# Kernel optimization log

Measured on AMD Instinct MI355X. Metric: run time of the kernel, lower is better.

## Reference

```python
import jax, jax.numpy as jnp
import numpy as np

SIGMA = 0.1
B = 1.0
SPATIAL_WEIGHT = 0.5
EPS = 1e-5


def setup_inputs() -> dict:
    key = jax.random.key(0)
    k1, k2 = jax.random.split(key)
    N, C, H, W = 2, 256, 64, 64
    I_features = jax.random.normal(k1, (N, C, H, W), dtype=jnp.float32)
    T_features = jax.random.normal(k2, (N, C, H, W), dtype=jnp.float32)
    return {"I_features": I_features, "T_features": T_features}


def _calc_cx(raw):
    # raw: [N, P_T, H, W]; min + exp-softmax over the target-patch axis (axis=1)
    mn = jnp.min(raw, axis=1, keepdims=True)
    rel = raw / (mn + EPS)
    w = jnp.exp((B - rel) / SIGMA)
    return w / jnp.sum(w, axis=1, keepdims=True)


def reference(I_features, T_features):
    N, C, H, W = I_features.shape
    P = H * W

    # ---- spatial branch: L2 distances on a normalized meshgrid (C=2) ----
    rows = jnp.arange(H, dtype=jnp.float32) / (H + 1)
    cols = jnp.arange(W, dtype=jnp.float32) / (W + 1)
    grid = jnp.stack(jnp.meshgrid(rows, cols, indexing="ij"))  # [2, H, W]
    g = grid.reshape(2, P)                                      # [2, P]
    sq = jnp.sum(g * g, axis=0)                                 # [P]
    d = sq[:, None] + sq[None, :] - 2.0 * (g.T @ g)             # [P_I, P_T]
    d = jnp.clip(d, 0.0)
    raw_sp = d.T.reshape(1, P, H, W)  # [1, P_T, H, W]; identical per sample
    cx_sp = _calc_cx(raw_sp)

    # ---- feature branch: cosine similarity via centered, L2-normed feats ----
    meanT = jnp.mean(T_features, axis=(0, 2, 3), keepdims=True)
    Ic = I_features - meanT
    Tc = T_features - meanT
    In = Ic / jnp.linalg.norm(Ic, axis=1, keepdims=True)
    Tn = Tc / jnp.linalg.norm(Tc, axis=1, keepdims=True)
    Iv = In.reshape(N, C, P)
    Tv = Tn.reshape(N, C, P)
    dot = jnp.einsum("ncq,ncp->nqp", Tv, Iv)  # [N, P_T, P_I]
    raw_feat = ((1.0 - dot) / 2.0).reshape(N, P, H, W)
    cx_feat = _calc_cx(raw_feat)

    # ---- combine, max over I positions, mean over T patches, -log, mean ----
    cx = (1.0 - SPATIAL_WEIGHT) * cx_feat + SPATIAL_WEIGHT * cx_sp  # [N,P,H,W]
    m = jnp.max(cx, axis=(2, 3))  # [N, P]
    m = jnp.mean(m, axis=1)       # [N]
    return jnp.mean(-jnp.log(m))
```

## Files before the change

### kernel.cpp

```cpp
#include <hip/hip_runtime.h>
#include <math.h>

#define PP 4096
#define CC 256
#define NN 2
#define NSTEP 16

typedef __attribute__((ext_vector_type(4))) float f32x4;

__device__ __forceinline__ void gld_lds16(const char* g, char* l) {
    __builtin_amdgcn_global_load_lds(
        (const __attribute__((address_space(1))) unsigned int*)g,
        (__attribute__((address_space(3))) unsigned int*)l, 16, 0, 0);
}


__global__ __launch_bounds__(256) void mean_kernel(const float* __restrict__ T,
                                                   float* __restrict__ meanT,
                                                   float* __restrict__ loss_acc) {
    int c = blockIdx.x, tid = threadIdx.x;
    float s = 0.f;
    for (int n = 0; n < NN; n++) {
        const float4* Tc = (const float4*)&T[(size_t)(n * CC + c) * PP];
        for (int g = 0; g < 4; g++) {
            float4 v = Tc[tid + g * 256];
            s += (v.x + v.y) + (v.z + v.w);
        }
    }
    __shared__ float red[256];
    red[tid] = s; __syncthreads();
    for (int st = 128; st > 0; st >>= 1) {
        if (tid < st) red[tid] += red[tid + st];
        __syncthreads();
    }
    if (tid == 0) meanT[c] = red[0] * (1.0f / (NN * PP));
    if (blockIdx.x == 0 && tid < NN) loss_acc[tid] = 0.f;
}

__global__ __launch_bounds__(256) void normalize_kernel(const float* __restrict__ I,
                                                        const float* __restrict__ T,
                                                        const float* __restrict__ meanT,
                                                        char* __restrict__ InT,
                                                        char* __restrict__ TnT) {
    int pc = blockIdx.x * 32;
    int n = blockIdx.y;
    int which = blockIdx.z;
    const float* X = which ? T : I;
    char* Y = which ? TnT : InT;

    __shared__ float tile[CC][36];
    __shared__ float red[32][32];
    __shared__ float invn[32];

    int tid = threadIdx.x;
    int pl4 = tid & 7, c0 = tid >> 3;
    float sq0 = 0.f, sq1 = 0.f, sq2 = 0.f, sq3 = 0.f;
    for (int c = c0; c < CC; c += 32) {
        float m = meanT[c];
        float4 v = *(const float4*)&X[(size_t)(n * CC + c) * PP + pc + pl4 * 4];
        v.x -= m; v.y -= m; v.z -= m; v.w -= m;
        *(float4*)&tile[c][pl4 * 4] = v;
        sq0 += v.x * v.x; sq1 += v.y * v.y; sq2 += v.z * v.z; sq3 += v.w * v.w;
    }
    red[c0][pl4 * 4 + 0] = sq0;
    red[c0][pl4 * 4 + 1] = sq1;
    red[c0][pl4 * 4 + 2] = sq2;
    red[c0][pl4 * 4 + 3] = sq3;
    __syncthreads();
    if (tid < 32) {
        float s = 0.f;
        for (int k = 0; k < 32; k++) s += red[k][tid];
        invn[tid] = 1.0f / sqrtf(s);
    }
    __syncthreads();
    for (int pass = 0; pass < 8; pass++) {
        int r = pass * 4 + (tid >> 6);
        int c4 = (tid & 63) * 4;
        float in = invn[r];
        float v0 = tile[c4 + 0][r] * in;
        float v1 = tile[c4 + 1][r] * in;
        float v2 = tile[c4 + 2][r] * in;
        float v3 = tile[c4 + 3][r] * in;
        int w = __builtin_amdgcn_cvt_pk_fp8_f32(v0, v1, 0, false);
        w = __builtin_amdgcn_cvt_pk_fp8_f32(v2, v3, w, true);
        *(unsigned*)&Y[(size_t)(n * PP + pc + r) * CC + c4] = (unsigned)w;
    }
}

__global__ __launch_bounds__(512) void cx_strip(const char* __restrict__ TnT,
                                                const char* __restrict__ InT,
                                                float* __restrict__ loss_acc) {
    const int strip = blockIdx.x;
    const int n = blockIdx.y;
    const int p0 = strip * 32;
    const char* __restrict__ Ab = TnT + (size_t)n * PP * CC;
    const char* __restrict__ Bb = InT + (size_t)n * PP * CC + (size_t)p0 * CC;

    __shared__ __align__(16) char Aw[8][2][8192];
    __shared__ __align__(16) char Bsm[8192];
    __shared__ float redw[8][32];
    __shared__ float inv2s[32];
    __shared__ float dwl[32];

    const int tid = threadIdx.x;
    const int l = tid & 63, wv = tid >> 6;
    const int lm = l & 15, quad = l >> 4;
    const int lr4 = l >> 4;
    const int sl = l & 15;

#define STAGE_A(qs, b)                                                       \
    {                                                                        \
        const char* sbase_ = Ab + ((size_t)(qs) * 256 + wv * 32) * 256;      \
        char* dbase_ = &Aw[wv][b][0];                                        \
        _Pragma("unroll")                                                    \
        for (int g_ = 0; g_ < 8; g_++) {                                     \
            int row_ = g_ * 4 + lr4;                                         \
            gld_lds16(sbase_ + row_ * 256 + ((sl ^ (row_ & 15)) * 16),       \
                      dbase_ + g_ * 1024);                                   \
        }                                                                    \
    }

    {
        int rB = wv * 4 + lr4;
        gld_lds16(Bb + rB * 256 + ((sl ^ (rB & 15)) * 16), &Bsm[wv * 1024]);
    }
    STAGE_A(0, 0);
    __syncthreads();

    long bf[2][8];
#pragma unroll
    for (int ct = 0; ct < 2; ct++)
#pragma unroll
        for (int ks = 0; ks < 8; ks++) {
            int g8 = ks * 4 + quad;
            int row = ct * 16 + lm;
            bf[ct][ks] = *(const long*)&Bsm[row * 256 +
                          (((g8 >> 1) ^ (row & 15)) * 16) + (g8 & 1) * 8];
        }

    float cm[2] = {3.4e38f, 3.4e38f};
    float inv2[2] = {0.f, 0.f};
    float ss[2] = {0.f, 0.f};
    const int qd = p0 >> 8;
    const int wd = (p0 >> 5) & 7;

#pragma unroll 1
    for (int pass = 0; pass < 2; pass++) {
        if (pass == 1) STAGE_A(0, 0);
#pragma unroll 1
        for (int qs = 0; qs < NSTEP; qs++) {
            if (qs < NSTEP - 1) {
                STAGE_A(qs + 1, (qs + 1) & 1);
                asm volatile("s_waitcnt vmcnt(8)" ::: "memory");
            } else {
                asm volatile("s_waitcnt vmcnt(0)" ::: "memory");
            }
            __builtin_amdgcn_sched_barrier(0);

            const char* Ac = &Aw[wv][qs & 1][0];
            f32x4 acc[2][2] = {};
#pragma unroll
            for (int ks = 0; ks < 8; ks++) {
                const int off = (((ks * 2 + (quad >> 1)) ^ lm) * 16) + (quad & 1) * 8;
                long a[2];
#pragma unroll
                for (int i = 0; i < 2; i++)
                    a[i] = *(const long*)&Ac[(i * 16 + lm) * 256 + off];
#pragma unroll
                for (int i = 0; i < 2; i++)
#pragma unroll
                    for (int ct = 0; ct < 2; ct++)
                        acc[i][ct] = __builtin_amdgcn_mfma_f32_16x16x32_fp8_fp8(
                            a[i], bf[ct][ks], acc[i][ct], 0, 0, 0);
            }
            if (pass == 0) {
#pragma unroll
                for (int ct = 0; ct < 2; ct++)
#pragma unroll
                    for (int i = 0; i < 2; i++)
#pragma unroll
                        for (int e = 0; e < 4; e++)
                            cm[ct] = fminf(cm[ct], (1.0f - acc[i][ct][e]) * 0.5f);
            } else {
                const bool dstep = (qs == qd) && (wv == wd);
#pragma unroll
                for (int ct = 0; ct < 2; ct++) {
                    float s2 = 0.f;
#pragma unroll
                    for (int i = 0; i < 2; i++)
#pragma unroll
                        for (int e = 0; e < 4; e++) {
                            float raw = (1.0f - acc[i][ct][e]) * 0.5f;
                            float w = exp2f(fmaf(raw, -inv2[ct], 14.4269504f));
                            s2 += w;
                            if (dstep && (i * 16 + quad * 4 + e == ct * 16 + lm))
                                dwl[ct * 16 + lm] = w;
                        }
                    ss[ct] += s2;
                }
            }
        }

        if (pass == 0) {
#pragma unroll
            for (int ct = 0; ct < 2; ct++) {
                cm[ct] = fminf(cm[ct], __shfl_xor(cm[ct], 16));
                cm[ct] = fminf(cm[ct], __shfl_xor(cm[ct], 32));
                if (quad == 0) redw[wv][ct * 16 + lm] = cm[ct];
            }
            __syncthreads();
            if (tid < 32) {
                float m = redw[0][tid];
#pragma unroll
                for (int w2 = 1; w2 < 8; w2++) m = fminf(m, redw[w2][tid]);
                inv2s[tid] = 14.4269504f / (m + 1e-5f);
            }
            __syncthreads();
            inv2[0] = inv2s[lm];
            inv2[1] = inv2s[16 + lm];
        }
    }

#pragma unroll
    for (int ct = 0; ct < 2; ct++) {
        ss[ct] += __shfl_xor(ss[ct], 16);
        ss[ct] += __shfl_xor(ss[ct], 32);
        if (quad == 0) redw[wv][ct * 16 + lm] = ss[ct];
    }
    __syncthreads();
    if (tid < 32) {
        float s = 0.f;
#pragma unroll
        for (int w2 = 0; w2 < 8; w2++) s += redw[w2][tid];
        float part = dwl[tid] / s;
        part += __shfl_xor(part, 1);
        part += __shfl_xor(part, 2);
        part += __shfl_xor(part, 4);
        part += __shfl_xor(part, 8);
        part += __shfl_xor(part, 16);
        if (tid == 0) atomicAdd(&loss_acc[n], part);
    }
#undef STAGE_A
}

__global__ void finalize_kernel(const float* __restrict__ loss_acc,
                                float* __restrict__ out) {
    float m0 = 0.5f + 0.5f * (loss_acc[0] / (float)PP);
    float m1 = 0.5f + 0.5f * (loss_acc[1] / (float)PP);
    out[0] = 0.5f * (-logf(m0) - logf(m1));
}

extern "C" void kernel_launch(void* const* d_in, const int* in_sizes, int n_in,
                              void* d_out, int out_size, void* d_ws, size_t ws_size,
                              hipStream_t stream) {
    const float* I = (const float*)d_in[0];
    const float* T = (const float*)d_in[1];
    float* out = (float*)d_out;

    char* ws = (char*)d_ws;
    const size_t SZ_F8 = (size_t)NN * PP * CC;
    char* InT = ws;
    char* TnT = ws + SZ_F8;
    float* meanT = (float*)(ws + 2 * SZ_F8);
    float* loss_acc = (float*)(ws + 2 * SZ_F8 + 32768);

    mean_kernel<<<CC, 256, 0, stream>>>(T, meanT, loss_acc);
    normalize_kernel<<<dim3(PP / 32, NN, 2), 256, 0, stream>>>(I, T, meanT, InT, TnT);
    cx_strip<<<dim3(PP / 32, NN), 512, 0, stream>>>(TnT, InT, loss_acc);
    finalize_kernel<<<1, 1, 0, stream>>>(loss_acc, out);
}
```

Measured before the change: 114.6 us.

## Use 16x16x128 scaled FP8 MFMA and fold raw-distance math into exp constants

Replaces the eight 16x16x32 FP8 MFMAs per k-step with two 16x16x128 scaled MFMA calls, using a unit scale, so fewer matrix instructions are issued. A-tile LDS offsets and global source pointers are precomputed once rather than recomputed every step. The min of raw distance becomes a max of the dot product, and the (1-x)/2 transform is folded into per-column exp2 constants, which removes per-element arithmetic and simplifies the diagonal capture. This uses more registers for the precomputed offsets and the wider operands.

```diff
diff --git a/kernel.cpp b/kernel.cpp
--- a/kernel.cpp
+++ b/kernel.cpp
@@ -7,6 +7,7 @@
 #define NSTEP 16
 
 typedef __attribute__((ext_vector_type(4))) float f32x4;
+typedef __attribute__((ext_vector_type(8))) int i32x8;
 
 __device__ __forceinline__ void gld_lds16(const char* g, char* l) {
     __builtin_amdgcn_global_load_lds(
@@ -108,17 +109,30 @@
     const int lr4 = l >> 4;
     const int sl = l & 15;
 
-#define STAGE_A(qs, b)                                                       \
-    {                                                                        \
-        const char* sbase_ = Ab + ((size_t)(qs) * 256 + wv * 32) * 256;      \
-        char* dbase_ = &Aw[wv][b][0];                                        \
-        _Pragma("unroll")                                                    \
-        for (int g_ = 0; g_ < 8; g_++) {                                     \
-            int row_ = g_ * 4 + lr4;                                         \
-            gld_lds16(sbase_ + row_ * 256 + ((sl ^ (row_ & 15)) * 16),       \
-                      dbase_ + g_ * 1024);                                   \
-        }                                                                    \
-    }
+    const char* asrc[8];
+#pragma unroll
+    for (int g = 0; g < 8; g++) {
+        int row = g * 4 + lr4;
+        asrc[g] = Ab + (size_t)(wv * 32 + row) * 256 + ((sl ^ (row & 15)) * 16);
+    }
+#define STAGE_A(qs, b)                                                        \
+    {                                                                         \
+        char* dbase_ = &Aw[wv][b][0];                                         \
+        _Pragma("unroll")                                                     \
+        for (int g_ = 0; g_ < 8; g_++)                                        \
+            gld_lds16(asrc[g_] + (size_t)(qs) * 65536, dbase_ + g_ * 1024);   \
+    }
+
+    int aoff[16];
+#pragma unroll
+    for (int i = 0; i < 2; i++)
+#pragma unroll
+        for (int kb = 0; kb < 2; kb++)
+#pragma unroll
+            for (int j = 0; j < 4; j++)
+                aoff[i * 8 + kb * 4 + j] =
+                    (i * 16 + lm) * 256 +
+                    (((kb * 8 + j * 2 + (quad >> 1)) ^ lm) * 16) + (quad & 1) * 8;
 
     {
         int rB = wv * 4 + lr4;
@@ -127,19 +141,19 @@
     STAGE_A(0, 0);
     __syncthreads();
 
-    long bf[2][8];
+    union BU { long l[2][8]; i32x8 v[2][2]; } bfu;
 #pragma unroll
     for (int ct = 0; ct < 2; ct++)
 #pragma unroll
         for (int ks = 0; ks < 8; ks++) {
             int g8 = ks * 4 + quad;
             int row = ct * 16 + lm;
-            bf[ct][ks] = *(const long*)&Bsm[row * 256 +
-                          (((g8 >> 1) ^ (row & 15)) * 16) + (g8 & 1) * 8];
-        }
-
-    float cm[2] = {3.4e38f, 3.4e38f};
-    float inv2[2] = {0.f, 0.f};
+            bfu.l[ct][ks] = *(const long*)&Bsm[row * 256 +
+                             (((g8 >> 1) ^ (row & 15)) * 16) + (g8 & 1) * 8];
+        }
+
+    float amax[2] = {-3.4e38f, -3.4e38f};
+    float hc[2] = {0.f, 0.f}, c0c[2] = {0.f, 0.f};
     float ss[2] = {0.f, 0.f};
     const int qd = p0 >> 8;
     const int wd = (p0 >> 5) & 7;
@@ -160,18 +174,22 @@
             const char* Ac = &Aw[wv][qs & 1][0];
             f32x4 acc[2][2] = {};
 #pragma unroll
-            for (int ks = 0; ks < 8; ks++) {
-                const int off = (((ks * 2 + (quad >> 1)) ^ lm) * 16) + (quad & 1) * 8;
-                long a[2];
+            for (int kb = 0; kb < 2; kb++) {
+                union AU { long l[4]; i32x8 v; } a_[2];
+#pragma unroll
+                for (int j = 0; j < 4; j++)
+#pragma unroll
+                    for (int i = 0; i < 2; i++)
+                        a_[i].l[j] = *(const long*)&Ac[aoff[i * 8 + kb * 4 + j]];
 #pragma unroll
                 for (int i = 0; i < 2; i++)
-                    a[i] = *(const long*)&Ac[(i * 16 + lm) * 256 + off];
-#pragma unroll
-                for (int i = 0; i < 2; i++)
 #pragma unroll
                     for (int ct = 0; ct < 2; ct++)
-                        acc[i][ct] = __builtin_amdgcn_mfma_f32_16x16x32_fp8_fp8(
-                            a[i], bf[ct][ks], acc[i][ct], 0, 0, 0);
+                        acc[i][ct] = __builtin_amdgcn_mfma_scale_f32_16x16x128_f8f6f4(
+                            a_[i].v, bfu.v[ct][kb], acc[i][ct],
+                            0, 0,
+                            0, 0x7f7f7f7f,
+                            0, 0x7f7f7f7f);
             }
             if (pass == 0) {
 #pragma unroll
@@ -180,44 +198,49 @@
                     for (int i = 0; i < 2; i++)
 #pragma unroll
                         for (int e = 0; e < 4; e++)
-                            cm[ct] = fminf(cm[ct], (1.0f - acc[i][ct][e]) * 0.5f);
+                            amax[ct] = fmaxf(amax[ct], acc[i][ct][e]);
             } else {
-                const bool dstep = (qs == qd) && (wv == wd);
 #pragma unroll
                 for (int ct = 0; ct < 2; ct++) {
                     float s2 = 0.f;
 #pragma unroll
                     for (int i = 0; i < 2; i++)
 #pragma unroll
-                        for (int e = 0; e < 4; e++) {
-                            float raw = (1.0f - acc[i][ct][e]) * 0.5f;
-                            float w = exp2f(fmaf(raw, -inv2[ct], 14.4269504f));
-                            s2 += w;
-                            if (dstep && (i * 16 + quad * 4 + e == ct * 16 + lm))
-                                dwl[ct * 16 + lm] = w;
-                        }
+                        for (int e = 0; e < 4; e++)
+                            s2 += exp2f(fmaf(acc[i][ct][e], hc[ct], c0c[ct]));
                     ss[ct] += s2;
                 }
+                if ((qs == qd) && (wv == wd)) {
+#pragma unroll
+                    for (int ct = 0; ct < 2; ct++)
+                        if (quad == (lm >> 2))
+                            dwl[ct * 16 + lm] = exp2f(
+                                fmaf(acc[ct][ct][lm & 3], hc[ct], c0c[ct]));
+                }
             }
         }
 
         if (pass == 0) {
 #pragma unroll
             for (int ct = 0; ct < 2; ct++) {
-                cm[ct] = fminf(cm[ct], __shfl_xor(cm[ct], 16));
-                cm[ct] = fminf(cm[ct], __shfl_xor(cm[ct], 32));
-                if (quad == 0) redw[wv][ct * 16 + lm] = cm[ct];
+                amax[ct] = fmaxf(amax[ct], __shfl_xor(amax[ct], 16));
+                amax[ct] = fmaxf(amax[ct], __shfl_xor(amax[ct], 32));
+                if (quad == 0) redw[wv][ct * 16 + lm] = amax[ct];
             }
             __syncthreads();
             if (tid < 32) {
-                float m = redw[0][tid];
-#pragma unroll
-                for (int w2 = 1; w2 < 8; w2++) m = fminf(m, redw[w2][tid]);
-                inv2s[tid] = 14.4269504f / (m + 1e-5f);
+                float mx = redw[0][tid];
+#pragma unroll
+                for (int w2 = 1; w2 < 8; w2++) mx = fmaxf(mx, redw[w2][tid]);
+                float mnv = (1.0f - mx) * 0.5f;
+                inv2s[tid] = 14.4269504f / (mnv + 1e-5f);
             }
             __syncthreads();
-            inv2[0] = inv2s[lm];
-            inv2[1] = inv2s[16 + lm];
+            {
+                float i20 = inv2s[lm], i21 = inv2s[16 + lm];
+                hc[0] = i20 * 0.5f; c0c[0] = 14.4269504f - hc[0];
+                hc[1] = i21 * 0.5f; c0c[1] = 14.4269504f - hc[1];
+            }
         }
     }
 
```

Measured after the change: 108.2 us. -5.6%, faster.
